# Optimization experiments

Hardware: AMD Instinct MI355X
Metric: run time of the kernel (lower is better)

The kernel has to match this reference:

```python
import jax, jax.numpy as jnp
import numpy as np

K = 16  # nsample


def _conv2d(x, w, b=None):
    # 1x1 conv2d: x [B,Cin,K,N], w [Cout,Cin]
    y = jnp.einsum('oc,bckn->bokn', w, x)
    return y if b is None else y + b[None, :, None, None]


def setup_inputs() -> dict:
    key = jax.random.key(0)
    ks = jax.random.split(key, 20)
    B, N1, N2, C = 2, 4096, 8192, 64
    Cin = C + 3  # in_channel + 3
    w = lambda k, shape, fan: (jax.random.normal(k, shape, jnp.float32) / np.sqrt(fan).astype(np.float32))
    return {
        'xyz1': jax.random.normal(ks[0], (B, 3, N1), jnp.float32),
        'xyz2': jax.random.normal(ks[1], (B, 3, N2), jnp.float32),
        'points1': jax.random.normal(ks[2], (B, C, N1), jnp.float32),
        'points2': jax.random.normal(ks[3], (B, C, N2), jnp.float32),
        'w_r0': w(ks[4], (C, Cin), Cin), 'b_r0': jnp.zeros((C,), jnp.float32),
        'w_r1': w(ks[5], (C, C), C), 'b_r1': jnp.zeros((C,), jnp.float32),
        'w_z0': w(ks[6], (C, Cin), Cin), 'b_z0': jnp.zeros((C,), jnp.float32),
        'w_z1': w(ks[7], (C, C), C), 'b_z1': jnp.zeros((C,), jnp.float32),
        'w_h0': w(ks[8], (C, Cin), Cin), 'b_h0': jnp.zeros((C,), jnp.float32),
        'w_h1': w(ks[9], (C, C), C), 'b_h1': jnp.zeros((C,), jnp.float32),
        'w_fuse_r': w(ks[10], (C, C), C),
        'w_fuse_z': w(ks[11], (C, C), C),
        'w_fuse_ro': w(ks[12], (C, C), C),
    }


def reference(xyz1, xyz2, points1, points2,
              w_r0, b_r0, w_r1, b_r1,
              w_z0, b_z0, w_z1, b_z1,
              w_h0, b_h0, w_h1, b_h1,
              w_fuse_r, w_fuse_z, w_fuse_ro):
    x1 = jnp.transpose(xyz1, (0, 2, 1))  # [B,N1,3]
    x2 = jnp.transpose(xyz2, (0, 2, 1))  # [B,N2,3]
    # squared pairwise distances [B,N1,N2]
    sq = (jnp.sum(x1 * x1, -1)[:, :, None]
          + jnp.sum(x2 * x2, -1)[:, None, :]
          - 2.0 * jnp.einsum('bnd,bmd->bnm', x1, x2))
    _, knn = jax.lax.top_k(-sq, K)  # [B,N1,K] smallest distances
    gather = jax.vmap(lambda p, i: p[i])
    nbr_xyz = gather(x2, knn)                 # [B,N1,K,3]
    dir_xyz = nbr_xyz - x1[:, :, None, :]
    p2 = gather(jnp.transpose(points2, (0, 2, 1)), knn)  # [B,N1,K,C]
    new_pts = jnp.transpose(jnp.concatenate([p2, dir_xyz], -1), (0, 3, 2, 1))  # [B,C+3,K,N1]

    lrelu = lambda v: jax.nn.leaky_relu(v, 0.1)
    fuse = lambda w, p: jnp.einsum('oc,bcn->bon', w, p)

    # r gate
    r = _conv2d(new_pts, w_r0, b_r0) + fuse(w_fuse_r, points1)[:, :, None, :]
    r = lrelu(r)
    r = jax.nn.sigmoid(_conv2d(r, w_r1, b_r1))  # [B,C,K,N1]

    # z gate (max over neighbors before last conv)
    z = _conv2d(new_pts, w_z0, b_z0) + fuse(w_fuse_z, points1)[:, :, None, :]
    z = lrelu(z)
    z = jnp.max(z, axis=2, keepdims=True)
    z = jax.nn.sigmoid(_conv2d(z, w_z1, b_z1))[:, :, 0, :]  # [B,C,N1]

    # h candidate
    p1e = _conv2d(r * points1[:, :, None, :], w_fuse_ro)
    h = lrelu(_conv2d(new_pts, w_h0, b_h0) + p1e)
    h = jnp.max(h, axis=2, keepdims=True)
    h = jnp.tanh(_conv2d(h, w_h1, b_h1))[:, :, 0, :]  # [B,C,N1]

    return (1.0 - z) * points1 + z * h
```

## Files before the change

kernel.cpp:

```cpp
#include <hip/hip_runtime.h>
#include <math.h>

typedef __attribute__((ext_vector_type(8))) short bf8_t;
typedef __attribute__((ext_vector_type(4))) float f32x4;

#define NB   2
#define N1S  4096
#define N2S  8192
#define CC   64
#define KK   16
#define GQ   4

#define M_R0 0
#define M_Z0 1
#define M_H0 2
#define M_R1 3
#define M_Z1 4
#define M_H1 5
#define M_FR 6
#define M_FZ 7
#define M_FRO 8

#define WA_SHORTS   (9*4*2*64*8)
#define WDIR_OFF    (WA_SHORTS*2)
#define WDIR_FLOATS (3*3*64)
#define XP_OFF      (WDIR_OFF + WDIR_FLOATS*4)
#define XP_BYTES    (NB*N2S*16)
#define KIDX_OFF    (XP_OFF + XP_BYTES)
#define KIDX_BYTES  (NB*N1S*KK*4)
#define P2B_OFF     (KIDX_OFF + KIDX_BYTES)
#define P2B_BYTES   ((size_t)NB*N2S*CC*2)

__device__ __forceinline__ float lrelu(float v){ return v > 0.f ? v : 0.1f*v; }
__device__ __forceinline__ float sigm(float v){ return 1.f/(1.f + __expf(-v)); }
__device__ __forceinline__ float tanh_(float v){ return 1.f - 2.f/(__expf(2.f*v) + 1.f); }
__device__ __forceinline__ unsigned short f2bf(float f){
  union { float f; unsigned u; } v; v.f = f;
  unsigned r = v.u + 0x7FFF + ((v.u >> 16) & 1);
  return (unsigned short)(r >> 16);
}

__global__ __launch_bounds__(256) void prep_misc(
    const float* __restrict__ points2,
    const float* __restrict__ r0, const float* __restrict__ z0, const float* __restrict__ h0,
    const float* __restrict__ r1, const float* __restrict__ z1, const float* __restrict__ h1,
    const float* __restrict__ fr, const float* __restrict__ fz, const float* __restrict__ fro,
    short* __restrict__ wa, float* __restrict__ wdir, unsigned short* __restrict__ p2b)
{
  __shared__ float t[64][65];
  const int blk = blockIdx.x;
  if (blk < 256) {
    const int b = blk >> 7; const int j0 = (blk & 127)*64;
    const int tx = threadIdx.x & 63; const int r4 = threadIdx.x >> 6;
    #pragma unroll
    for (int c = r4; c < 64; c += 4) t[c][tx] = points2[((size_t)b*CC + c)*N2S + j0 + tx];
    __syncthreads();
    #pragma unroll
    for (int j = r4; j < 64; j += 4) p2b[((size_t)b*N2S + j0 + j)*CC + tx] = f2bf(t[tx][j]);
  } else {
    const float* W[9] = {r0, z0, h0, r1, z1, h1, fr, fz, fro};
    const int Ks[9]   = {67, 67, 67, 64, 64, 64, 64, 64, 64};
    for (int i = (blk - 256)*256 + threadIdx.x; i < WA_SHORTS; i += 16*256) {
      const int j = i & 7, l = (i >> 3) & 63, kk = (i >> 9) & 1, r = (i >> 10) & 3, mat = i >> 12;
      const int row = r*16 + (l & 15);
      const int c = kk*32 + ((l >> 4) << 3) + j;
      wa[i] = (short)f2bf(W[mat][row*Ks[mat] + c]);
    }
    for (int i = (blk - 256)*256 + threadIdx.x; i < WDIR_FLOATS; i += 16*256) {
      const int g = i / 192, rem = i % 192, d = rem / 64, o = rem & 63;
      wdir[i] = W[g][o*67 + 64 + d];
    }
  }
}

__global__ __launch_bounds__(256) void pack_xyz2(const float* __restrict__ xyz2, float4* __restrict__ xp){
  const int i = blockIdx.x*256 + threadIdx.x;
  const int b = i >> 13, j = i & (N2S-1);
  const float x = xyz2[((size_t)(b*3+0))*N2S + j];
  const float y = xyz2[((size_t)(b*3+1))*N2S + j];
  const float z = xyz2[((size_t)(b*3+2))*N2S + j];
  xp[i] = make_float4(x, y, z, (x*x + y*y) + z*z);
}

__global__ __launch_bounds__(256) void knn_kernel(
    const float* __restrict__ xyz1, const float4* __restrict__ xp, int* __restrict__ idxout)
{
  __shared__ float pdL[4][2][16];
  __shared__ int   piL[4][2][16];
  const int tid = threadIdx.x, w = tid >> 6, lane = tid & 63, grp = lane >> 4;
  const int qbase = blockIdx.x*4;
  const int b = qbase >> 12;
  const int q0 = qbase + (w >> 1)*2;
  const int half = w & 1;
  const int hbase = half*(N2S/2);
  const float4* __restrict__ X = xp + (b << 13);
  float qx[2], qy[2], qz[2], s1[2], kth[2], kappa[2], m[2];
  #pragma unroll
  for (int g = 0; g < 2; g++) {
    const int n = (q0 + g) & (N1S-1);
    qx[g] = xyz1[((size_t)(b*3+0))*N1S + n];
    qy[g] = xyz1[((size_t)(b*3+1))*N1S + n];
    qz[g] = xyz1[((size_t)(b*3+2))*N1S + n];
    s1[g] = (qx[g]*qx[g] + qy[g]*qy[g]) + qz[g]*qz[g];
    kth[g] = INFINITY; m[g] = INFINITY;
  }

  #pragma unroll 2
  for (int c0 = 0; c0 < N2S/2; c0 += 256) {
    const float4 v0 = X[hbase + c0 + lane];
    const float4 v1 = X[hbase + c0 + 64 + lane];
    const float4 v2 = X[hbase + c0 + 128 + lane];
    const float4 v3 = X[hbase + c0 + 192 + lane];
    #pragma unroll
    for (int g = 0; g < 2; g++) {
      const float d0 = (s1[g] + v0.w) - 2.f*((qx[g]*v0.x + qy[g]*v0.y) + qz[g]*v0.z);
      const float d1 = (s1[g] + v1.w) - 2.f*((qx[g]*v1.x + qy[g]*v1.y) + qz[g]*v1.z);
      const float d2 = (s1[g] + v2.w) - 2.f*((qx[g]*v2.x + qy[g]*v2.y) + qz[g]*v2.z);
      const float d3 = (s1[g] + v3.w) - 2.f*((qx[g]*v3.x + qy[g]*v3.y) + qz[g]*v3.z);
      m[g] = fminf(m[g], fminf(fminf(d0, d1), fminf(d2, d3)));
    }
  }
  #pragma unroll
  for (int g = 0; g < 2; g++) {
    float v = m[g];
    #pragma unroll
    for (int k = 2; k <= 64; k <<= 1) {
      #pragma unroll
      for (int j = k >> 1; j > 0; j >>= 1) {
        const float pv = __shfl_xor(v, j);
        const bool up = ((lane & k) == 0);
        const bool keepmin = up ? ((lane & j) == 0) : ((lane & j) != 0);
        v = keepmin ? fminf(v, pv) : fmaxf(v, pv);
      }
    }
    kappa[g] = __shfl(v, 16);
  }

  float listd = INFINITY; int listi = 0;
  #pragma unroll 2
  for (int c0 = 0; c0 < N2S/2; c0 += 64) {
    const float4 v = X[hbase + c0 + lane];
    #pragma unroll
    for (int g = 0; g < 2; g++) {
      const float d = (s1[g] + v.w) - 2.f*((qx[g]*v.x + qy[g]*v.y) + qz[g]*v.z);
      unsigned long long vote = __ballot(d < fminf(kth[g], kappa[g]));
      while (vote) {
        const int src = (int)__builtin_ctzll(vote);
        vote &= vote - 1;
        const float dv = __shfl(d, src);
        if (dv < kth[g]) {
          const int iv = hbase + c0 + src;
          const float ud = __shfl_up(listd, 1);
          const int   ui = __shfl_up(listi, 1);
          const bool ing = (grp == g);
          const bool cm = ing && (dv < listd);
          const bool cp = cm && ((lane & 15) > 0) && (dv < ud);
          listd = cm ? (cp ? ud : dv) : listd;
          listi = cm ? (cp ? ui : iv) : listi;
          kth[g] = __shfl(listd, g*16 + 15);
        }
      }
    }
  }

  {
    bool need = false;
    #pragma unroll
    for (int g = 0; g < 2; g++) need = need || (kth[g] == INFINITY);
    if (__builtin_expect(need, 0)) {
      #pragma unroll
      for (int g = 0; g < 2; g++) {
        if (kth[g] == INFINITY) {
          if (grp == g) { listd = INFINITY; listi = 0; }
          float kk2 = INFINITY;
          for (int c0 = 0; c0 < N2S/2; c0 += 64) {
            const float4 v = X[hbase + c0 + lane];
            const float d = (s1[g] + v.w) - 2.f*((qx[g]*v.x + qy[g]*v.y) + qz[g]*v.z);
            unsigned long long vote = __ballot(d < kk2);
            while (vote) {
              const int src = (int)__builtin_ctzll(vote);
              vote &= vote - 1;
              const float dv = __shfl(d, src);
              if (dv < kk2) {
                const int iv = hbase + c0 + src;
                const float ud = __shfl_up(listd, 1);
                const int   ui = __shfl_up(listi, 1);
                const bool ing = (grp == g);
                const bool cm = ing && (dv < listd);
                const bool cp = cm && ((lane & 15) > 0) && (dv < ud);
                listd = cm ? (cp ? ud : dv) : listd;
                listi = cm ? (cp ? ui : iv) : listi;
                kk2 = __shfl(listd, g*16 + 15);
              }
            }
          }
        }
      }
    }
  }

  if (grp < 2) {
    const int qi = (w >> 1)*2 + grp;
    pdL[qi][half][lane & 15] = listd;
    piL[qi][half][lane & 15] = listi;
  }
  __syncthreads();

  {
    float d = (lane < 32) ? pdL[w][lane >> 4][lane & 15] : INFINITY;
    int   i = (lane < 32) ? piL[w][lane >> 4][lane & 15] : 0x7fffffff;
    #pragma unroll
    for (int k = 2; k <= 64; k <<= 1) {
      #pragma unroll
      for (int j = k >> 1; j > 0; j >>= 1) {
        const float pdv = __shfl_xor(d, j);
        const int   piv = __shfl_xor(i, j);
        const bool keepmin = (((lane & k) == 0) == ((lane & j) == 0));
        const bool ownless = (d < pdv) || (d == pdv && i < piv);
        const bool takeown = keepmin ? ownless : !ownless;
        d = takeown ? d : pdv;
        i = takeown ? i : piv;
      }
    }
    if (lane < KK) idxout[(size_t)(qbase + w)*KK + lane] = i;
  }
}

#define FRAG(mat, kk) (*(const bf8_t*)(wA + (((mat)*4 + w)*2 + (kk))*512 + lane*8))

__global__ __launch_bounds__(256) void gates_kernel(
    const float* __restrict__ xyz1, const float* __restrict__ xyz2,
    const float* __restrict__ points1, const unsigned short* __restrict__ p2b,
    const int* __restrict__ kidx, const short* __restrict__ wA,
    const float* __restrict__ wdir,
    const float* __restrict__ b_r0, const float* __restrict__ b_z0,
    const float* __restrict__ b_h0, const float* __restrict__ b_r1,
    const float* __restrict__ b_z1, const float* __restrict__ b_h1,
    float* __restrict__ out)
{
  __shared__ __align__(16) short featB[2][GQ][64][8];
  __shared__ __align__(16) short rB[2][GQ][64][8];
  __shared__ __align__(16) float p1f[64][GQ];
  __shared__ __align__(16) short p1B[2][64][8];
  __shared__ float BFr[64][GQ], BFz[64][GQ];
  __shared__ float zmaxL[64][GQ], hmaxL[64][GQ];
  __shared__ float biasL[6][64];
  __shared__ float dirL[3][GQ*KK];
  __shared__ __align__(16) float obuf[64][GQ];

  const int tid = threadIdx.x;
  const int w = tid >> 6, lane = tid & 63;
  const int b  = blockIdx.x >> 10;
  const int n0 = (blockIdx.x & 1023) * GQ;
  const int cq = lane & 15;
  const int reg_o0 = w*16 + ((lane >> 4) << 2);
  const f32x4 zero4 = {0.f, 0.f, 0.f, 0.f};

  for (int i = tid; i < 6*64; i += 256) {
    const int a = i >> 6, o = i & 63;
    const float* bp = (a==0)?b_r0:(a==1)?b_z0:(a==2)?b_h0:(a==3)?b_r1:(a==4)?b_z1:b_h1;
    biasL[a][o] = bp[o];
  }
  if (tid < 64) {
    const float* sp = points1 + ((size_t)(b*CC + tid))*N1S + n0;
    *(float4*)&p1f[tid][0] = ((const float4*)sp)[0];
  }
  ((unsigned long long*)&p1B[0][0][0])[tid] = 0ULL;
  if (tid < 64) {
    const int m = tid, qg = n0 + (m >> 4);
    const int j = kidx[(size_t)((b << 12) + qg)*KK + (m & 15)];
    #pragma unroll
    for (int d = 0; d < 3; d++)
      dirL[d][m] = xyz2[((size_t)(b*3+d))*N2S + j] - xyz1[((size_t)(b*3+d))*N1S + qg];
  }
  {
    const int m = tid >> 2, qt = tid & 3;
    const int ct = m >> 4;
    const int qg = n0 + ct;
    const int j = kidx[(size_t)((b << 12) + qg)*KK + (m & 15)];
    const uint4* __restrict__ src = (const uint4*)(p2b + (((size_t)(b << 13) + j)*CC + qt*16));
    const uint4 u0 = src[0], u1 = src[1];
    *(uint4*)&featB[qt >> 1][ct][((qt & 1)*2 + 0)*16 + (m & 15)][0] = u0;
    *(uint4*)&featB[qt >> 1][ct][((qt & 1)*2 + 1)*16 + (m & 15)][0] = u1;
  }
  __syncthreads();

  {
    const int s0 = tid*4;
    const int j0 = s0 & 7, l = (s0 >> 3) & 63, kk = s0 >> 9;
    const int q = l & 15;
    if (q < GQ) {
      unsigned short t0[4];
      #pragma unroll
      for (int jj = 0; jj < 4; jj++)
        t0[jj] = f2bf(p1f[kk*32 + ((l >> 4) << 3) + j0 + jj][q]);
      uint2 pk; pk.x = t0[0] | ((unsigned)t0[1] << 16); pk.y = t0[2] | ((unsigned)t0[3] << 16);
      *(uint2*)&p1B[kk][l][j0] = pk;
    }
  }
  __syncthreads();

  {
    const bf8_t fa0 = FRAG(M_FR, 0), fa1 = FRAG(M_FR, 1);
    const bf8_t ga0 = FRAG(M_FZ, 0), ga1 = FRAG(M_FZ, 1);
    const bf8_t pb0 = *(const bf8_t*)&p1B[0][lane][0];
    const bf8_t pb1 = *(const bf8_t*)&p1B[1][lane][0];
    f32x4 ar = __builtin_amdgcn_mfma_f32_16x16x32_bf16(fa0, pb0, zero4, 0, 0, 0);
    ar = __builtin_amdgcn_mfma_f32_16x16x32_bf16(fa1, pb1, ar, 0, 0, 0);
    f32x4 az = __builtin_amdgcn_mfma_f32_16x16x32_bf16(ga0, pb0, zero4, 0, 0, 0);
    az = __builtin_amdgcn_mfma_f32_16x16x32_bf16(ga1, pb1, az, 0, 0, 0);
    if (cq < GQ) {
      #pragma unroll
      for (int r2 = 0; r2 < 4; r2++) {
        const int o = reg_o0 + r2;
        BFr[o][cq] = ar[r2] + biasL[0][o];
        BFz[o][cq] = az[r2] + biasL[1][o];
      }
    }
  }

  {
    const bf8_t ra0 = FRAG(M_R0, 0), ra1 = FRAG(M_R0, 1);
    const bf8_t za0 = FRAG(M_Z0, 0), za1 = FRAG(M_Z0, 1);
    float wdr[3][4], wdz[3][4];
    #pragma unroll
    for (int d = 0; d < 3; d++)
      #pragma unroll
      for (int r2 = 0; r2 < 4; r2++) {
        wdr[d][r2] = wdir[(0*3 + d)*64 + reg_o0 + r2];
        wdz[d][r2] = wdir[(1*3 + d)*64 + reg_o0 + r2];
      }
    const int kkv = reg_o0 >> 5, lp = ((reg_o0 & 31) >> 3)*16 + cq, j0 = reg_o0 & 7;
    #pragma unroll
    for (int ct = 0; ct < GQ; ct++) {
      const bf8_t fb0 = *(const bf8_t*)&featB[0][ct][lane][0];
      const bf8_t fb1 = *(const bf8_t*)&featB[1][ct][lane][0];
      f32x4 accr = __builtin_amdgcn_mfma_f32_16x16x32_bf16(ra0, fb0, zero4, 0, 0, 0);
      accr = __builtin_amdgcn_mfma_f32_16x16x32_bf16(ra1, fb1, accr, 0, 0, 0);
      f32x4 accz = __builtin_amdgcn_mfma_f32_16x16x32_bf16(za0, fb0, zero4, 0, 0, 0);
      accz = __builtin_amdgcn_mfma_f32_16x16x32_bf16(za1, fb1, accz, 0, 0, 0);
      const int m = ct*16 + cq;
      const float d0 = dirL[0][m], d1 = dirL[1][m], d2 = dirL[2][m];
      unsigned short rpk[4]; float zv[4];
      #pragma unroll
      for (int r2 = 0; r2 < 4; r2++) {
        const int o = reg_o0 + r2;
        float rv = accr[r2] + BFr[o][ct] + wdr[0][r2]*d0 + wdr[1][r2]*d1 + wdr[2][r2]*d2;
        rpk[r2] = f2bf(lrelu(rv));
        float zt = accz[r2] + BFz[o][ct] + wdz[0][r2]*d0 + wdz[1][r2]*d1 + wdz[2][r2]*d2;
        zv[r2] = lrelu(zt);
      }
      uint2 pk; pk.x = rpk[0] | ((unsigned)rpk[1] << 16); pk.y = rpk[2] | ((unsigned)rpk[3] << 16);
      *(uint2*)&rB[kkv][ct][lp][j0] = pk;
      #pragma unroll
      for (int r2 = 0; r2 < 4; r2++) {
        float vv = zv[r2];
        vv = fmaxf(vv, __shfl_xor(vv, 1));
        vv = fmaxf(vv, __shfl_xor(vv, 2));
        vv = fmaxf(vv, __shfl_xor(vv, 4));
        vv = fmaxf(vv, __shfl_xor(vv, 8));
        zv[r2] = vv;
      }
      if (cq == 0) {
        #pragma unroll
        for (int r2 = 0; r2 < 4; r2++) zmaxL[reg_o0 + r2][ct] = zv[r2];
      }
    }
  }
  __syncthreads();

  uint2 rpK[GQ];
  float zg[4];
  {
    const bf8_t r1a0 = FRAG(M_R1, 0), r1a1 = FRAG(M_R1, 1);
    #pragma unroll
    for (int ct = 0; ct < GQ; ct++) {
      const bf8_t b0 = *(const bf8_t*)&rB[0][ct][lane][0];
      const bf8_t b1 = *(const bf8_t*)&rB[1][ct][lane][0];
      f32x4 acc = __builtin_amdgcn_mfma_f32_16x16x32_bf16(r1a0, b0, zero4, 0, 0, 0);
      acc = __builtin_amdgcn_mfma_f32_16x16x32_bf16(r1a1, b1, acc, 0, 0, 0);
      unsigned short pk4[4];
      #pragma unroll
      for (int r2 = 0; r2 < 4; r2++) {
        const int o = reg_o0 + r2;
        const float rg = sigm(acc[r2] + biasL[3][o]);
        pk4[r2] = f2bf(rg * p1f[o][ct]);
      }
      rpK[ct].x = pk4[0] | ((unsigned)pk4[1] << 16);
      rpK[ct].y = pk4[2] | ((unsigned)pk4[3] << 16);
    }
    const bf8_t z1a0 = FRAG(M_Z1, 0), z1a1 = FRAG(M_Z1, 1);
    const int qc = cq < GQ ? cq : (GQ-1);
    bf8_t zb0, zb1;
    #pragma unroll
    for (int j = 0; j < 8; j++) {
      zb0[j] = (short)f2bf(zmaxL[((lane >> 4) << 3) + j][qc]);
      zb1[j] = (short)f2bf(zmaxL[32 + ((lane >> 4) << 3) + j][qc]);
    }
    f32x4 az = __builtin_amdgcn_mfma_f32_16x16x32_bf16(z1a0, zb0, zero4, 0, 0, 0);
    az = __builtin_amdgcn_mfma_f32_16x16x32_bf16(z1a1, zb1, az, 0, 0, 0);
    #pragma unroll
    for (int r2 = 0; r2 < 4; r2++) zg[r2] = sigm(az[r2] + biasL[4][reg_o0 + r2]);
  }
  __syncthreads();

  {
    const int kkv = reg_o0 >> 5, lp = ((reg_o0 & 31) >> 3)*16 + cq, j0 = reg_o0 & 7;
    #pragma unroll
    for (int ct = 0; ct < GQ; ct++) *(uint2*)&rB[kkv][ct][lp][j0] = rpK[ct];
  }
  __syncthreads();

  {
    const bf8_t h0a0 = FRAG(M_H0, 0), h0a1 = FRAG(M_H0, 1);
    const bf8_t foa0 = FRAG(M_FRO, 0), foa1 = FRAG(M_FRO, 1);
    float wdh[3][4];
    #pragma unroll
    for (int d = 0; d < 3; d++)
      #pragma unroll
      for (int r2 = 0; r2 < 4; r2++) wdh[d][r2] = wdir[(2*3 + d)*64 + reg_o0 + r2];
    #pragma unroll
    for (int ct = 0; ct < GQ; ct++) {
      const bf8_t fb0 = *(const bf8_t*)&featB[0][ct][lane][0];
      const bf8_t fb1 = *(const bf8_t*)&featB[1][ct][lane][0];
      const bf8_t rb0 = *(const bf8_t*)&rB[0][ct][lane][0];
      const bf8_t rb1 = *(const bf8_t*)&rB[1][ct][lane][0];
      f32x4 acc = __builtin_amdgcn_mfma_f32_16x16x32_bf16(h0a0, fb0, zero4, 0, 0, 0);
      acc = __builtin_amdgcn_mfma_f32_16x16x32_bf16(h0a1, fb1, acc, 0, 0, 0);
      acc = __builtin_amdgcn_mfma_f32_16x16x32_bf16(foa0, rb0, acc, 0, 0, 0);
      acc = __builtin_amdgcn_mfma_f32_16x16x32_bf16(foa1, rb1, acc, 0, 0, 0);
      const int m = ct*16 + cq;
      const float d0 = dirL[0][m], d1 = dirL[1][m], d2 = dirL[2][m];
      float hv[4];
      #pragma unroll
      for (int r2 = 0; r2 < 4; r2++) {
        const int o = reg_o0 + r2;
        hv[r2] = lrelu(acc[r2] + biasL[2][o] + wdh[0][r2]*d0 + wdh[1][r2]*d1 + wdh[2][r2]*d2);
      }
      #pragma unroll
      for (int r2 = 0; r2 < 4; r2++) {
        float vv = hv[r2];
        vv = fmaxf(vv, __shfl_xor(vv, 1));
        vv = fmaxf(vv, __shfl_xor(vv, 2));
        vv = fmaxf(vv, __shfl_xor(vv, 4));
        vv = fmaxf(vv, __shfl_xor(vv, 8));
        hv[r2] = vv;
      }
      if (cq == 0) {
        #pragma unroll
        for (int r2 = 0; r2 < 4; r2++) hmaxL[reg_o0 + r2][ct] = hv[r2];
      }
    }
  }
  __syncthreads();

  {
    const bf8_t h1a0 = FRAG(M_H1, 0), h1a1 = FRAG(M_H1, 1);
    const int qc = cq < GQ ? cq : (GQ-1);
    bf8_t hb0, hb1;
    #pragma unroll
    for (int j = 0; j < 8; j++) {
      hb0[j] = (short)f2bf(hmaxL[((lane >> 4) << 3) + j][qc]);
      hb1[j] = (short)f2bf(hmaxL[32 + ((lane >> 4) << 3) + j][qc]);
    }
    f32x4 ah = __builtin_amdgcn_mfma_f32_16x16x32_bf16(h1a0, hb0, zero4, 0, 0, 0);
    ah = __builtin_amdgcn_mfma_f32_16x16x32_bf16(h1a1, hb1, ah, 0, 0, 0);
    if (cq < GQ) {
      #pragma unroll
      for (int r2 = 0; r2 < 4; r2++) {
        const int o = reg_o0 + r2;
        const float hg = tanh_(ah[r2] + biasL[5][o]);
        obuf[o][cq] = (1.f - zg[r2])*p1f[o][cq] + zg[r2]*hg;
      }
    }
  }
  __syncthreads();
  if (tid < 64)
    *(float4*)(out + ((size_t)(b*CC + tid))*N1S + n0) = *(float4*)&obuf[tid][0];
}

extern "C" void kernel_launch(void* const* d_in, const int* in_sizes, int n_in,
                              void* d_out, int out_size, void* d_ws, size_t ws_size,
                              hipStream_t stream) {
  const float* xyz1    = (const float*)d_in[0];
  const float* xyz2    = (const float*)d_in[1];
  const float* points1 = (const float*)d_in[2];
  const float* points2 = (const float*)d_in[3];
  const float* w_r0 = (const float*)d_in[4];
  const float* b_r0 = (const float*)d_in[5];
  const float* w_r1 = (const float*)d_in[6];
  const float* b_r1 = (const float*)d_in[7];
  const float* w_z0 = (const float*)d_in[8];
  const float* b_z0 = (const float*)d_in[9];
  const float* w_z1 = (const float*)d_in[10];
  const float* b_z1 = (const float*)d_in[11];
  const float* w_h0 = (const float*)d_in[12];
  const float* b_h0 = (const float*)d_in[13];
  const float* w_h1 = (const float*)d_in[14];
  const float* b_h1 = (const float*)d_in[15];
  const float* w_fr  = (const float*)d_in[16];
  const float* w_fz  = (const float*)d_in[17];
  const float* w_fro = (const float*)d_in[18];
  float* out = (float*)d_out;

  short*  wa   = (short*)d_ws;
  float*  wdir = (float*)((char*)d_ws + WDIR_OFF);
  float4* xp   = (float4*)((char*)d_ws + XP_OFF);
  int*    kidx = (int*)((char*)d_ws + KIDX_OFF);
  unsigned short* p2b = (unsigned short*)((char*)d_ws + P2B_OFF);

  prep_misc<<<272, 256, 0, stream>>>(points2,
                                     w_r0, w_z0, w_h0, w_r1, w_z1, w_h1,
                                     w_fr, w_fz, w_fro, wa, wdir, p2b);
  pack_xyz2<<<64, 256, 0, stream>>>(xyz2, xp);

  knn_kernel<<<2048, 256, 0, stream>>>(xyz1, xp, kidx);

  gates_kernel<<<2048, 256, 0, stream>>>(
      xyz1, xyz2, points1, p2b, kidx, wa, wdir,
      b_r0, b_z0, b_h0, b_r1, b_z1, b_h1, out);
}
```

Baseline: 192.2 us.

## Fuse kNN search into gates kernel, passing neighbor indices through shared memory

Merges the kNN kernel and the gates kernel into one launch. Each block first finds the 16 nearest neighbours for its 4 queries, then stores the indices in shared memory instead of a global buffer, and the gate computation reads them from there. This removes a kernel launch, the global write and read of the index array, and the workspace for it. In exchange the fused kernel uses more registers and shared memory, which may lower occupancy, and the kNN phase and the MFMA gate phase can no longer overlap across separate kernels.

```diff
diff --git a/kernel.cpp b/kernel.cpp
--- a/kernel.cpp
+++ b/kernel.cpp
@@ -26,9 +26,7 @@
 #define WDIR_FLOATS (3*3*64)
 #define XP_OFF      (WDIR_OFF + WDIR_FLOATS*4)
 #define XP_BYTES    (NB*N2S*16)
-#define KIDX_OFF    (XP_OFF + XP_BYTES)
-#define KIDX_BYTES  (NB*N1S*KK*4)
-#define P2B_OFF     (KIDX_OFF + KIDX_BYTES)
+#define P2B_OFF     (XP_OFF + XP_BYTES)
 #define P2B_BYTES   ((size_t)NB*N2S*CC*2)
 
 __device__ __forceinline__ float lrelu(float v){ return v > 0.f ? v : 0.1f*v; }
@@ -82,162 +80,21 @@
   xp[i] = make_float4(x, y, z, (x*x + y*y) + z*z);
 }
 
-__global__ __launch_bounds__(256) void knn_kernel(
-    const float* __restrict__ xyz1, const float4* __restrict__ xp, int* __restrict__ idxout)
-{
-  __shared__ float pdL[4][2][16];
-  __shared__ int   piL[4][2][16];
-  const int tid = threadIdx.x, w = tid >> 6, lane = tid & 63, grp = lane >> 4;
-  const int qbase = blockIdx.x*4;
-  const int b = qbase >> 12;
-  const int q0 = qbase + (w >> 1)*2;
-  const int half = w & 1;
-  const int hbase = half*(N2S/2);
-  const float4* __restrict__ X = xp + (b << 13);
-  float qx[2], qy[2], qz[2], s1[2], kth[2], kappa[2], m[2];
-  #pragma unroll
-  for (int g = 0; g < 2; g++) {
-    const int n = (q0 + g) & (N1S-1);
-    qx[g] = xyz1[((size_t)(b*3+0))*N1S + n];
-    qy[g] = xyz1[((size_t)(b*3+1))*N1S + n];
-    qz[g] = xyz1[((size_t)(b*3+2))*N1S + n];
-    s1[g] = (qx[g]*qx[g] + qy[g]*qy[g]) + qz[g]*qz[g];
-    kth[g] = INFINITY; m[g] = INFINITY;
-  }
-
-  #pragma unroll 2
-  for (int c0 = 0; c0 < N2S/2; c0 += 256) {
-    const float4 v0 = X[hbase + c0 + lane];
-    const float4 v1 = X[hbase + c0 + 64 + lane];
-    const float4 v2 = X[hbase + c0 + 128 + lane];
-    const float4 v3 = X[hbase + c0 + 192 + lane];
-    #pragma unroll
-    for (int g = 0; g < 2; g++) {
-      const float d0 = (s1[g] + v0.w) - 2.f*((qx[g]*v0.x + qy[g]*v0.y) + qz[g]*v0.z);
-      const float d1 = (s1[g] + v1.w) - 2.f*((qx[g]*v1.x + qy[g]*v1.y) + qz[g]*v1.z);
-      const float d2 = (s1[g] + v2.w) - 2.f*((qx[g]*v2.x + qy[g]*v2.y) + qz[g]*v2.z);
-      const float d3 = (s1[g] + v3.w) - 2.f*((qx[g]*v3.x + qy[g]*v3.y) + qz[g]*v3.z);
-      m[g] = fminf(m[g], fminf(fminf(d0, d1), fminf(d2, d3)));
-    }
-  }
-  #pragma unroll
-  for (int g = 0; g < 2; g++) {
-    float v = m[g];
-    #pragma unroll
-    for (int k = 2; k <= 64; k <<= 1) {
-      #pragma unroll
-      for (int j = k >> 1; j > 0; j >>= 1) {
-        const float pv = __shfl_xor(v, j);
-        const bool up = ((lane & k) == 0);
-        const bool keepmin = up ? ((lane & j) == 0) : ((lane & j) != 0);
-        v = keepmin ? fminf(v, pv) : fmaxf(v, pv);
-      }
-    }
-    kappa[g] = __shfl(v, 16);
-  }
-
-  float listd = INFINITY; int listi = 0;
-  #pragma unroll 2
-  for (int c0 = 0; c0 < N2S/2; c0 += 64) {
-    const float4 v = X[hbase + c0 + lane];
-    #pragma unroll
-    for (int g = 0; g < 2; g++) {
-      const float d = (s1[g] + v.w) - 2.f*((qx[g]*v.x + qy[g]*v.y) + qz[g]*v.z);
-      unsigned long long vote = __ballot(d < fminf(kth[g], kappa[g]));
-      while (vote) {
-        const int src = (int)__builtin_ctzll(vote);
-        vote &= vote - 1;
-        const float dv = __shfl(d, src);
-        if (dv < kth[g]) {
-          const int iv = hbase + c0 + src;
-          const float ud = __shfl_up(listd, 1);
-          const int   ui = __shfl_up(listi, 1);
-          const bool ing = (grp == g);
-          const bool cm = ing && (dv < listd);
-          const bool cp = cm && ((lane & 15) > 0) && (dv < ud);
-          listd = cm ? (cp ? ud : dv) : listd;
-          listi = cm ? (cp ? ui : iv) : listi;
-          kth[g] = __shfl(listd, g*16 + 15);
-        }
-      }
-    }
-  }
-
-  {
-    bool need = false;
-    #pragma unroll
-    for (int g = 0; g < 2; g++) need = need || (kth[g] == INFINITY);
-    if (__builtin_expect(need, 0)) {
-      #pragma unroll
-      for (int g = 0; g < 2; g++) {
-        if (kth[g] == INFINITY) {
-          if (grp == g) { listd = INFINITY; listi = 0; }
-          float kk2 = INFINITY;
-          for (int c0 = 0; c0 < N2S/2; c0 += 64) {
-            const float4 v = X[hbase + c0 + lane];
-            const float d = (s1[g] + v.w) - 2.f*((qx[g]*v.x + qy[g]*v.y) + qz[g]*v.z);
-            unsigned long long vote = __ballot(d < kk2);
-            while (vote) {
-              const int src = (int)__builtin_ctzll(vote);
-              vote &= vote - 1;
-              const float dv = __shfl(d, src);
-              if (dv < kk2) {
-                const int iv = hbase + c0 + src;
-                const float ud = __shfl_up(listd, 1);
-                const int   ui = __shfl_up(listi, 1);
-                const bool ing = (grp == g);
-                const bool cm = ing && (dv < listd);
-                const bool cp = cm && ((lane & 15) > 0) && (dv < ud);
-                listd = cm ? (cp ? ud : dv) : listd;
-                listi = cm ? (cp ? ui : iv) : listi;
-                kk2 = __shfl(listd, g*16 + 15);
-              }
-            }
-          }
-        }
-      }
-    }
-  }
-
-  if (grp < 2) {
-    const int qi = (w >> 1)*2 + grp;
-    pdL[qi][half][lane & 15] = listd;
-    piL[qi][half][lane & 15] = listi;
-  }
-  __syncthreads();
-
-  {
-    float d = (lane < 32) ? pdL[w][lane >> 4][lane & 15] : INFINITY;
-    int   i = (lane < 32) ? piL[w][lane >> 4][lane & 15] : 0x7fffffff;
-    #pragma unroll
-    for (int k = 2; k <= 64; k <<= 1) {
-      #pragma unroll
-      for (int j = k >> 1; j > 0; j >>= 1) {
-        const float pdv = __shfl_xor(d, j);
-        const int   piv = __shfl_xor(i, j);
-        const bool keepmin = (((lane & k) == 0) == ((lane & j) == 0));
-        const bool ownless = (d < pdv) || (d == pdv && i < piv);
-        const bool takeown = keepmin ? ownless : !ownless;
-        d = takeown ? d : pdv;
-        i = takeown ? i : piv;
-      }
-    }
-    if (lane < KK) idxout[(size_t)(qbase + w)*KK + lane] = i;
-  }
-}
-
 #define FRAG(mat, kk) (*(const bf8_t*)(wA + (((mat)*4 + w)*2 + (kk))*512 + lane*8))
 
-__global__ __launch_bounds__(256) void gates_kernel(
-    const float* __restrict__ xyz1, const float* __restrict__ xyz2,
-    const float* __restrict__ points1, const unsigned short* __restrict__ p2b,
-    const int* __restrict__ kidx, const short* __restrict__ wA,
+__global__ __launch_bounds__(256) void knn_gates_kernel(
+    const float* __restrict__ xyz1, const float4* __restrict__ xp,
+    const float* __restrict__ xyz2, const float* __restrict__ points1,
+    const unsigned short* __restrict__ p2b, const short* __restrict__ wA,
     const float* __restrict__ wdir,
     const float* __restrict__ b_r0, const float* __restrict__ b_z0,
     const float* __restrict__ b_h0, const float* __restrict__ b_r1,
     const float* __restrict__ b_z1, const float* __restrict__ b_h1,
     float* __restrict__ out)
 {
+  __shared__ float pdL[4][2][16];
+  __shared__ int   piL[4][2][16];
+  __shared__ int   kidxL[4][16];
   __shared__ __align__(16) short featB[2][GQ][64][8];
   __shared__ __align__(16) short rB[2][GQ][64][8];
   __shared__ __align__(16) float p1f[64][GQ];
@@ -248,10 +105,149 @@
   __shared__ float dirL[3][GQ*KK];
   __shared__ __align__(16) float obuf[64][GQ];
 
-  const int tid = threadIdx.x;
-  const int w = tid >> 6, lane = tid & 63;
+  const int tid = threadIdx.x, w = tid >> 6, lane = tid & 63, grp = lane >> 4;
   const int b  = blockIdx.x >> 10;
   const int n0 = (blockIdx.x & 1023) * GQ;
+  const int qbase = blockIdx.x*4;
+
+  {
+    const int q0 = qbase + (w >> 1)*2;
+    const int half = w & 1;
+    const int hbase = half*(N2S/2);
+    const float4* __restrict__ X = xp + (b << 13);
+    float qx[2], qy[2], qz[2], s1[2], kth[2], kappa[2], m[2];
+    #pragma unroll
+    for (int g = 0; g < 2; g++) {
+      const int n = (q0 + g) & (N1S-1);
+      qx[g] = xyz1[((size_t)(b*3+0))*N1S + n];
+      qy[g] = xyz1[((size_t)(b*3+1))*N1S + n];
+      qz[g] = xyz1[((size_t)(b*3+2))*N1S + n];
+      s1[g] = (qx[g]*qx[g] + qy[g]*qy[g]) + qz[g]*qz[g];
+      kth[g] = INFINITY; m[g] = INFINITY;
+    }
+
+    #pragma unroll 2
+    for (int c0 = 0; c0 < N2S/2; c0 += 256) {
+      const float4 v0 = X[hbase + c0 + lane];
+      const float4 v1 = X[hbase + c0 + 64 + lane];
+      const float4 v2 = X[hbase + c0 + 128 + lane];
+      const float4 v3 = X[hbase + c0 + 192 + lane];
+      #pragma unroll
+      for (int g = 0; g < 2; g++) {
+        const float d0 = (s1[g] + v0.w) - 2.f*((qx[g]*v0.x + qy[g]*v0.y) + qz[g]*v0.z);
+        const float d1 = (s1[g] + v1.w) - 2.f*((qx[g]*v1.x + qy[g]*v1.y) + qz[g]*v1.z);
+        const float d2 = (s1[g] + v2.w) - 2.f*((qx[g]*v2.x + qy[g]*v2.y) + qz[g]*v2.z);
+        const float d3 = (s1[g] + v3.w) - 2.f*((qx[g]*v3.x + qy[g]*v3.y) + qz[g]*v3.z);
+        m[g] = fminf(m[g], fminf(fminf(d0, d1), fminf(d2, d3)));
+      }
+    }
+    #pragma unroll
+    for (int g = 0; g < 2; g++) {
+      float v = m[g];
+      #pragma unroll
+      for (int k = 2; k <= 64; k <<= 1) {
+        #pragma unroll
+        for (int j = k >> 1; j > 0; j >>= 1) {
+          const float pv = __shfl_xor(v, j);
+          const bool up = ((lane & k) == 0);
+          const bool keepmin = up ? ((lane & j) == 0) : ((lane & j) != 0);
+          v = keepmin ? fminf(v, pv) : fmaxf(v, pv);
+        }
+      }
+      kappa[g] = __shfl(v, 16);
+    }
+
+    float listd = INFINITY; int listi = 0;
+    #pragma unroll 2
+    for (int c0 = 0; c0 < N2S/2; c0 += 64) {
+      const float4 v = X[hbase + c0 + lane];
+      #pragma unroll
+      for (int g = 0; g < 2; g++) {
+        const float d = (s1[g] + v.w) - 2.f*((qx[g]*v.x + qy[g]*v.y) + qz[g]*v.z);
+        unsigned long long vote = __ballot(d < fminf(kth[g], kappa[g]));
+        while (vote) {
+          const int src = (int)__builtin_ctzll(vote);
+          vote &= vote - 1;
+          const float dv = __shfl(d, src);
+          if (dv < kth[g]) {
+            const int iv = hbase + c0 + src;
+            const float ud = __shfl_up(listd, 1);
+            const int   ui = __shfl_up(listi, 1);
+            const bool ing = (grp == g);
+            const bool cm = ing && (dv < listd);
+            const bool cp = cm && ((lane & 15) > 0) && (dv < ud);
+            listd = cm ? (cp ? ud : dv) : listd;
+            listi = cm ? (cp ? ui : iv) : listi;
+            kth[g] = __shfl(listd, g*16 + 15);
+          }
+        }
+      }
+    }
+
+    {
+      bool need = false;
+      #pragma unroll
+      for (int g = 0; g < 2; g++) need = need || (kth[g] == INFINITY);
+      if (__builtin_expect(need, 0)) {
+        #pragma unroll
+        for (int g = 0; g < 2; g++) {
+          if (kth[g] == INFINITY) {
+            if (grp == g) { listd = INFINITY; listi = 0; }
+            float kk2 = INFINITY;
+            for (int c0 = 0; c0 < N2S/2; c0 += 64) {
+              const float4 v = X[hbase + c0 + lane];
+              const float d = (s1[g] + v.w) - 2.f*((qx[g]*v.x + qy[g]*v.y) + qz[g]*v.z);
+              unsigned long long vote = __ballot(d < kk2);
+              while (vote) {
+                const int src = (int)__builtin_ctzll(vote);
+                vote &= vote - 1;
+                const float dv = __shfl(d, src);
+                if (dv < kk2) {
+                  const int iv = hbase + c0 + src;
+                  const float ud = __shfl_up(listd, 1);
+                  const int   ui = __shfl_up(listi, 1);
+                  const bool ing = (grp == g);
+                  const bool cm = ing && (dv < listd);
+                  const bool cp = cm && ((lane & 15) > 0) && (dv < ud);
+                  listd = cm ? (cp ? ud : dv) : listd;
+                  listi = cm ? (cp ? ui : iv) : listi;
+                  kk2 = __shfl(listd, g*16 + 15);
+                }
+              }
+            }
+          }
+        }
+      }
+    }
+
+    if (grp < 2) {
+      const int qi = (w >> 1)*2 + grp;
+      pdL[qi][half][lane & 15] = listd;
+      piL[qi][half][lane & 15] = listi;
+    }
+    __syncthreads();
+
+    {
+      float d = (lane < 32) ? pdL[w][lane >> 4][lane & 15] : INFINITY;
+      int   i = (lane < 32) ? piL[w][lane >> 4][lane & 15] : 0x7fffffff;
+      #pragma unroll
+      for (int k = 2; k <= 64; k <<= 1) {
+        #pragma unroll
+        for (int j = k >> 1; j > 0; j >>= 1) {
+          const float pdv = __shfl_xor(d, j);
+          const int   piv = __shfl_xor(i, j);
+          const bool keepmin = (((lane & k) == 0) == ((lane & j) == 0));
+          const bool ownless = (d < pdv) || (d == pdv && i < piv);
+          const bool takeown = keepmin ? ownless : !ownless;
+          d = takeown ? d : pdv;
+          i = takeown ? i : piv;
+        }
+      }
+      if (lane < KK) kidxL[w][lane] = i;
+    }
+  }
+  __syncthreads();
+
   const int cq = lane & 15;
   const int reg_o0 = w*16 + ((lane >> 4) << 2);
   const f32x4 zero4 = {0.f, 0.f, 0.f, 0.f};
@@ -268,7 +264,7 @@
   ((unsigned long long*)&p1B[0][0][0])[tid] = 0ULL;
   if (tid < 64) {
     const int m = tid, qg = n0 + (m >> 4);
-    const int j = kidx[(size_t)((b << 12) + qg)*KK + (m & 15)];
+    const int j = kidxL[m >> 4][m & 15];
     #pragma unroll
     for (int d = 0; d < 3; d++)
       dirL[d][m] = xyz2[((size_t)(b*3+d))*N2S + j] - xyz1[((size_t)(b*3+d))*N1S + qg];
@@ -276,8 +272,7 @@
   {
     const int m = tid >> 2, qt = tid & 3;
     const int ct = m >> 4;
-    const int qg = n0 + ct;
-    const int j = kidx[(size_t)((b << 12) + qg)*KK + (m & 15)];
+    const int j = kidxL[ct][m & 15];
     const uint4* __restrict__ src = (const uint4*)(p2b + (((size_t)(b << 13) + j)*CC + qt*16));
     const uint4 u0 = src[0], u1 = src[1];
     *(uint4*)&featB[qt >> 1][ct][((qt & 1)*2 + 0)*16 + (m & 15)][0] = u0;
@@ -506,7 +501,6 @@
   short*  wa   = (short*)d_ws;
   float*  wdir = (float*)((char*)d_ws + WDIR_OFF);
   float4* xp   = (float4*)((char*)d_ws + XP_OFF);
-  int*    kidx = (int*)((char*)d_ws + KIDX_OFF);
   unsigned short* p2b = (unsigned short*)((char*)d_ws + P2B_OFF);
 
   prep_misc<<<272, 256, 0, stream>>>(points2,
@@ -514,9 +508,7 @@
                                      w_fr, w_fz, w_fro, wa, wdir, p2b);
   pack_xyz2<<<64, 256, 0, stream>>>(xyz2, xp);
 
-  knn_kernel<<<2048, 256, 0, stream>>>(xyz1, xp, kidx);
-
-  gates_kernel<<<2048, 256, 0, stream>>>(
-      xyz1, xyz2, points1, p2b, kidx, wa, wdir,
+  knn_gates_kernel<<<2048, 256, 0, stream>>>(
+      xyz1, xp, xyz2, points1, p2b, wa, wdir,
       b_r0, b_z0, b_h0, b_r1, b_z1, b_h1, out);
 }
```

After: 190.0 us. Within noise of the previous version (-1.2%).
